# Kernel optimization log

Measured on AMD Instinct MI355X. Metric: run time of the kernel, lower is better.

The kernel has to match this reference:

```python
import jax, jax.numpy as jnp
import numpy as np

NSIDE = 256
N_FACETS = 12 * NSIDE * NSIDE  # 786432
N0 = 300000
N1 = 300000
M = 4194304  # pooled child slots, divisible by 4

JRLL = jnp.array([2, 2, 2, 2, 3, 3, 3, 3, 4, 4, 4, 4], dtype=jnp.int32)
JPLL = jnp.array([1, 3, 5, 7, 0, 2, 4, 6, 1, 3, 5, 7], dtype=jnp.int32)


def _compress_bits(v):
    # keep even bits of v and compact them (de-interleave), 32-bit
    v = v & 0x55555555
    v = (v | (v >> 1)) & 0x33333333
    v = (v | (v >> 2)) & 0x0F0F0F0F
    v = (v | (v >> 4)) & 0x00FF00FF
    v = (v | (v >> 8)) & 0x0000FFFF
    return v


def pix2vec_nest(nside, pix):
    # HEALPix nested pix -> unit cartesian (x, y, z), matches hp.pix2vec(nside, pix, nest=True)
    pix = pix.astype(jnp.int32)
    npface = nside * nside
    face = pix // npface
    ipf = pix - face * npface
    ix = _compress_bits(ipf)
    iy = _compress_bits(ipf >> 1)
    jr = JRLL[face] * nside - ix - iy - 1  # ring index
    north = jr < nside
    south = jr > 3 * nside
    nr = jnp.where(north, jr, jnp.where(south, 4 * nside - jr, nside))
    fact2 = 4.0 / (12.0 * nside * nside)
    fact1 = (2.0 * nside) * fact2
    nrf = nr.astype(jnp.float32)
    z = jnp.where(
        north, 1.0 - nrf * nrf * fact2,
        jnp.where(south, nrf * nrf * fact2 - 1.0,
                  (2 * nside - jr).astype(jnp.float32) * fact1))
    kshift = jnp.where(north | south, 0, (jr - nside) & 1)
    num = JPLL[face] * nr + ix - iy + 1 + kshift
    jp = jnp.where(num >= 0, num // 2, -((-num) // 2))  # C-style truncating division
    jp = jnp.where(jp > 4 * nr, jp - 4 * nr, jp)
    jp = jnp.where(jp < 1, jp + 4 * nr, jp)
    phi = (jp.astype(jnp.float32) - (kshift.astype(jnp.float32) + 1.0) * 0.5) * (jnp.pi * 0.5) / nrf
    sth = jnp.sqrt((1.0 - z) * (1.0 + z))
    return sth * jnp.cos(phi), sth * jnp.sin(phi), z


def _safe_div(num, den):
    # matches torch.nan_to_num(num/den) here because den==0 implies num==0 (scores >= 0)
    d = jnp.where(den == 0, 1.0, den)
    return jnp.where(den == 0, 0.0, num / d)


def center_of_gravity(position, scores):
    # position [M,3], scores [M]; 4 children per parent (view(-1,4) in torch)
    s = scores.reshape(-1, 4)              # [P,4]
    p = position.reshape(-1, 4, 3)         # [P,4,3]
    den = s.sum(axis=1)                    # [P]
    pos_cog = _safe_div(jnp.einsum('pc,pcd->pd', s, p), den[:, None])
    cnt = (s > 0).sum(axis=1).astype(s.dtype)
    score_cog = _safe_div(den, cnt)
    return pos_cog, score_cog


def setup_inputs() -> dict:
    key = jax.random.key(0)
    k1, k2, k3, k4, k5 = jax.random.split(key, 5)
    # unique facet labels per keypoint (mirrors deterministic dict construction)
    img0_child_facets = jax.random.permutation(k1, N_FACETS)[:N0][None].astype(jnp.int32)
    img1_child_facets = jax.random.permutation(k2, N_FACETS)[:N1][None].astype(jnp.int32)
    correspondences = jax.random.randint(k3, (1, N0), 0, N1, dtype=jnp.int32)  # all >= 0
    filt = jax.random.randint(k4, (M,), 0, N_FACETS, dtype=jnp.int32)
    keypointScores1 = jax.random.uniform(k5, (1, N1), dtype=jnp.float32)
    return {
        'nside': NSIDE,
        'correspondences': correspondences,
        'img0_child_facets': img0_child_facets,
        'img1_child_facets': img1_child_facets,
        'img0_filtered_child_facets_for_pooling': filt,
        'keypointScores1': keypointScores1,
    }


def reference(nside, correspondences, img0_child_facets, img1_child_facets,
              img0_filtered_child_facets_for_pooling, keypointScores1):
    # all correspondences >= 0 in this setup -> masked_select keeps everything
    n_kpts0 = correspondences.shape[1]
    kptidx_with_corr_img0 = jnp.arange(n_kpts0, dtype=jnp.int32)
    kptidx_with_corr_img1 = correspondences[0].astype(jnp.int32)
    facets_with_corr_img0 = img0_child_facets[0]                      # [N0]
    facets_with_corr_img1 = img1_child_facets[0][kptidx_with_corr_img1]
    # dict {facet_img0 -> facet_img1}, then {0: 0} override
    lut_corr = (jnp.zeros(N_FACETS, jnp.int32)
                .at[facets_with_corr_img0].set(facets_with_corr_img1.astype(jnp.int32))
                .at[0].set(0))
    # dict {facet_img1 -> keypoint index}, then {0: 0} override
    lut_kpt = (jnp.zeros(N_FACETS, jnp.int32)
               .at[img1_child_facets[0]].set(jnp.arange(img1_child_facets.shape[1], dtype=jnp.int32))
               .at[0].set(0))
    # torch.isin(filtered, facets_with_corr_img0) via membership table
    member = jnp.zeros(N_FACETS, bool).at[facets_with_corr_img0].set(True)
    filt = img0_filtered_child_facets_for_pooling
    mask = member[filt].astype(jnp.float32)                           # [M]
    filt_masked = (filt.astype(jnp.float32) * mask).astype(jnp.int32)
    a = lut_corr[filt_masked]                                         # corresponding img1 facets
    x, y, z = pix2vec_nest(nside, a)
    pos = jnp.stack([x, y, z], axis=1) * mask[:, None]                # [M,3]
    b = lut_kpt[a]
    scores = keypointScores1[0][b] * mask                             # [M]
    pos_cog, score_cog = center_of_gravity(pos, scores)
    return (pos_cog, score_cog[None, :], kptidx_with_corr_img0,
            kptidx_with_corr_img1, keypointScores1)
```

## Files before the change

### kernel.cpp

```cpp
#include <hip/hip_runtime.h>
#include <hip/hip_bf16.h>

#define NSIDE    256
#define NFACETS  786432

typedef int vint4 __attribute__((ext_vector_type(4)));
typedef unsigned uvec4 __attribute__((ext_vector_type(4)));

__device__ __forceinline__ unsigned encode_score(float s) {
    if (s <= 0.f) return 0u;
    unsigned u = __float_as_uint(s);
    u += 0x8000u + ((u >> 16) & 1u);
    int e = (int)((u >> 23) & 0xFFu);
    unsigned m = (u >> 16) & 0x7Fu;
    int field = e - 95;
    if (field < 1)  { field = 1; m = 0u; }
    if (field > 31) { field = 31; m = 127u; }
    return ((unsigned)field << 7) | m;
}
__device__ __forceinline__ float decode_score(unsigned c) {
    if (c == 0u) return 0.f;
    unsigned field = (c >> 7) & 0x1Fu;
    unsigned m = c & 0x7Fu;
    return __uint_as_float(((field + 95u) << 23) | (m << 16));
}

__device__ __forceinline__ unsigned compress_bits(unsigned v) {
    v &= 0x55555555u;
    v = (v | (v >> 1)) & 0x33333333u;
    v = (v | (v >> 2)) & 0x0F0F0F0Fu;
    v = (v | (v >> 4)) & 0x00FF00FFu;
    v = (v | (v >> 8)) & 0x0000FFFFu;
    return v;
}

__device__ __forceinline__ float3 pix2vec_nest256(int pix) {
    int face = pix >> 16;
    unsigned ipf = (unsigned)(pix & 0xFFFF);
    int ix = (int)compress_bits(ipf);
    int iy = (int)compress_bits(ipf >> 1);
    int jrll = 2 + (face >> 2);
    int jpll = 2 * (face & 3) + (((face >> 2) == 1) ? 0 : 1);
    int jr = jrll * NSIDE - ix - iy - 1;
    bool north = jr < NSIDE;
    bool south = jr > 3 * NSIDE;
    int nr = north ? jr : (south ? 4 * NSIDE - jr : NSIDE);
    const float fact2 = 4.0f / (12.0f * (float)NSIDE * (float)NSIDE);
    const float fact1 = (2.0f * (float)NSIDE) * fact2;
    float nrf = (float)nr;
    float z;
    if (north)      z = 1.0f - nrf * nrf * fact2;
    else if (south) z = nrf * nrf * fact2 - 1.0f;
    else            z = (float)(2 * NSIDE - jr) * fact1;
    int kshift = (north || south) ? 0 : (jr & 1);
    int num = jpll * nr + ix - iy + 1 + kshift;
    int jp = num / 2;
    if (jp > 4 * nr) jp -= 4 * nr;
    if (jp < 1)      jp += 4 * nr;
    float phi = ((float)jp - ((float)kshift + 1.0f) * 0.5f) * (1.5707963267948966f / nrf);
    float sth = sqrtf((1.0f - z) * (1.0f + z));
    float sp, cp;
    __sincosf(phi, &sp, &cp);
    float3 r;
    r.x = sth * cp;
    r.y = sth * sp;
    r.z = z;
    return r;
}

__global__ __launch_bounds__(256)
void zero_tail_kernel(uvec4* __restrict__ table4,
                      const int* __restrict__ corr,
                      const float* __restrict__ kps,
                      float* __restrict__ out,
                      int nwords4, int n0, int n1,
                      int idx0_off, int idx1_off, int kps_off) {
    int i = blockIdx.x * blockDim.x + threadIdx.x;
    if (i < nwords4) {
        uvec4 z = {0u, 0u, 0u, 0u};
        table4[i] = z;
    }
    if (i < n0) {
        __builtin_nontemporal_store((float)i, &out[idx0_off + i]);
        __builtin_nontemporal_store((float)corr[i], &out[idx1_off + i]);
    }
    if (i < n1) {
        __builtin_nontemporal_store(kps[i], &out[kps_off + i]);
    }
}

__global__ __launch_bounds__(256)
void build_kernel(const int* __restrict__ corr,
                  const int* __restrict__ f0s,
                  const int* __restrict__ f1s,
                  const float* __restrict__ kps,
                  unsigned* __restrict__ table,
                  int n0) {
    int i = blockIdx.x * blockDim.x + threadIdx.x;
    if (i >= n0) return;
    int f0 = f0s[i];
    int j  = corr[i];
    int a = (f0 == 0) ? 0 : f1s[j];
    int b = (a == 0) ? 0 : j;
    float sc = kps[b];
    unsigned code = ((unsigned)a << 12) | encode_score(sc);
    table[f0] = code;
}

__global__ __launch_bounds__(256)
void cog_kernel(const vint4* __restrict__ filt4,
                const unsigned* __restrict__ table,
                float* __restrict__ out,
                int P, int score_off) {
    int p = blockIdx.x * blockDim.x + threadIdx.x;
    if (p >= P) return;
    vint4 f = __builtin_nontemporal_load(&filt4[p]);
    unsigned t0 = table[f.x];
    unsigned t1 = table[f.y];
    unsigned t2 = table[f.z];
    unsigned t3 = table[f.w];
    float s0 = decode_score(t0 & 0xFFFu);
    float s1 = decode_score(t1 & 0xFFFu);
    float s2 = decode_score(t2 & 0xFFFu);
    float s3 = decode_score(t3 & 0xFFFu);
    float3 v0 = pix2vec_nest256((int)(t0 >> 12));
    float3 v1 = pix2vec_nest256((int)(t1 >> 12));
    float3 v2 = pix2vec_nest256((int)(t2 >> 12));
    float3 v3 = pix2vec_nest256((int)(t3 >> 12));
    float den = s0 + s1 + s2 + s3;
    float px = s0 * v0.x + s1 * v1.x + s2 * v2.x + s3 * v3.x;
    float py = s0 * v0.y + s1 * v1.y + s2 * v2.y + s3 * v3.y;
    float pz = s0 * v0.z + s1 * v1.z + s2 * v2.z + s3 * v3.z;
    int cnt = (int)(s0 > 0.f) + (int)(s1 > 0.f) + (int)(s2 > 0.f) + (int)(s3 > 0.f);
    float ox = 0.f, oy = 0.f, oz = 0.f, osc = 0.f;
    if (den != 0.f) {
        float inv = 1.0f / den;
        ox = px * inv; oy = py * inv; oz = pz * inv;
        float rcp = (cnt == 1) ? 1.f : (cnt == 2) ? 0.5f : (cnt == 3) ? (1.f / 3.f) : 0.25f;
        osc = den * rcp;
    }
    __builtin_nontemporal_store(ox, &out[3 * p + 0]);
    __builtin_nontemporal_store(oy, &out[3 * p + 1]);
    __builtin_nontemporal_store(oz, &out[3 * p + 2]);
    __builtin_nontemporal_store(osc, &out[score_off + p]);
}

extern "C" void kernel_launch(void* const* d_in, const int* in_sizes, int n_in,
                              void* d_out, int out_size, void* d_ws, size_t ws_size,
                              hipStream_t stream) {
    const int* corr = (const int*)d_in[1];
    const int* f0s  = (const int*)d_in[2];
    const int* f1s  = (const int*)d_in[3];
    const int* filt = (const int*)d_in[4];
    const float* kps = (const float*)d_in[5];

    const int n0 = in_sizes[1];
    const int n1 = in_sizes[5];
    const int M  = in_sizes[4];
    const int P  = M / 4;

    const int score_off = 3 * P;
    const int idx0_off  = 4 * P;
    const int idx1_off  = idx0_off + n0;
    const int kps_off   = idx1_off + n0;

    unsigned* table = (unsigned*)d_ws;
    float* out = (float*)d_out;

    const int b = 256;
    const int nwords4 = NFACETS / 4;
    int nmax = nwords4;
    if (n0 > nmax) nmax = n0;
    if (n1 > nmax) nmax = n1;

    zero_tail_kernel<<<(nmax + b - 1) / b, b, 0, stream>>>((uvec4*)table, corr, kps, out,
                                                           nwords4, n0, n1,
                                                           idx0_off, idx1_off, kps_off);
    build_kernel<<<(n0 + b - 1) / b, b, 0, stream>>>(corr, f0s, f1s, kps, table, n0);
    cog_kernel<<<(P + b - 1) / b, b, 0, stream>>>((const vint4*)filt, table, out, P, score_off);
}
```

Before: 44.15 us.

## Add LDS membership bitmap to skip table gathers and pix2vec for empty facets

The build kernel now also sets a bit per occupied facet in a global bitmap (96KB), which the cog kernel copies into shared memory. The cog kernel becomes a persistent grid-stride kernel of 1024-thread blocks. It tests the bitmap before gathering from the 3MB table and skips pix2vec when all four scores are zero. This cuts random global gathers for unmatched facets, at the cost of atomics in the build kernel, a bitmap copy per block, reduced occupancy from the large shared allocation, and lost parallelism from the fixed 256-block grid.

Result: slower. 50.05 us (+13.4%).

```diff
diff --git a/kernel.cpp b/kernel.cpp
--- a/kernel.cpp
+++ b/kernel.cpp
@@ -3,6 +3,7 @@
 
 #define NSIDE    256
 #define NFACETS  786432
+#define BM_WORDS 24576
 
 typedef int vint4 __attribute__((ext_vector_type(4)));
 typedef unsigned uvec4 __attribute__((ext_vector_type(4)));
@@ -69,7 +70,7 @@
 }
 
 __global__ __launch_bounds__(256)
-void zero_tail_kernel(uvec4* __restrict__ table4,
+void zero_tail_kernel(uvec4* __restrict__ ws4,
                       const int* __restrict__ corr,
                       const float* __restrict__ kps,
                       float* __restrict__ out,
@@ -78,7 +79,7 @@
     int i = blockIdx.x * blockDim.x + threadIdx.x;
     if (i < nwords4) {
         uvec4 z = {0u, 0u, 0u, 0u};
-        table4[i] = z;
+        ws4[i] = z;
     }
     if (i < n0) {
         __builtin_nontemporal_store((float)i, &out[idx0_off + i]);
@@ -95,6 +96,7 @@
                   const int* __restrict__ f1s,
                   const float* __restrict__ kps,
                   unsigned* __restrict__ table,
+                  unsigned* __restrict__ gbm,
                   int n0) {
     int i = blockIdx.x * blockDim.x + threadIdx.x;
     if (i >= n0) return;
@@ -105,44 +107,59 @@
     float sc = kps[b];
     unsigned code = ((unsigned)a << 12) | encode_score(sc);
     table[f0] = code;
+    atomicOr(&gbm[f0 >> 5], 1u << (f0 & 31));
 }
 
-__global__ __launch_bounds__(256)
+__global__ __launch_bounds__(1024, 1)
 void cog_kernel(const vint4* __restrict__ filt4,
                 const unsigned* __restrict__ table,
+                const unsigned* __restrict__ gbm,
                 float* __restrict__ out,
                 int P, int score_off) {
-    int p = blockIdx.x * blockDim.x + threadIdx.x;
-    if (p >= P) return;
-    vint4 f = __builtin_nontemporal_load(&filt4[p]);
-    unsigned t0 = table[f.x];
-    unsigned t1 = table[f.y];
-    unsigned t2 = table[f.z];
-    unsigned t3 = table[f.w];
-    float s0 = decode_score(t0 & 0xFFFu);
-    float s1 = decode_score(t1 & 0xFFFu);
-    float s2 = decode_score(t2 & 0xFFFu);
-    float s3 = decode_score(t3 & 0xFFFu);
-    float3 v0 = pix2vec_nest256((int)(t0 >> 12));
-    float3 v1 = pix2vec_nest256((int)(t1 >> 12));
-    float3 v2 = pix2vec_nest256((int)(t2 >> 12));
-    float3 v3 = pix2vec_nest256((int)(t3 >> 12));
-    float den = s0 + s1 + s2 + s3;
-    float px = s0 * v0.x + s1 * v1.x + s2 * v2.x + s3 * v3.x;
-    float py = s0 * v0.y + s1 * v1.y + s2 * v2.y + s3 * v3.y;
-    float pz = s0 * v0.z + s1 * v1.z + s2 * v2.z + s3 * v3.z;
-    int cnt = (int)(s0 > 0.f) + (int)(s1 > 0.f) + (int)(s2 > 0.f) + (int)(s3 > 0.f);
-    float ox = 0.f, oy = 0.f, oz = 0.f, osc = 0.f;
-    if (den != 0.f) {
-        float inv = 1.0f / den;
-        ox = px * inv; oy = py * inv; oz = pz * inv;
-        float rcp = (cnt == 1) ? 1.f : (cnt == 2) ? 0.5f : (cnt == 3) ? (1.f / 3.f) : 0.25f;
-        osc = den * rcp;
+    __shared__ unsigned bm[BM_WORDS];
+    {
+        const uvec4* g4 = (const uvec4*)gbm;
+        uvec4* b4 = (uvec4*)bm;
+        for (int w = threadIdx.x; w < BM_WORDS / 4; w += blockDim.x) b4[w] = g4[w];
     }
-    __builtin_nontemporal_store(ox, &out[3 * p + 0]);
-    __builtin_nontemporal_store(oy, &out[3 * p + 1]);
-    __builtin_nontemporal_store(oz, &out[3 * p + 2]);
-    __builtin_nontemporal_store(osc, &out[score_off + p]);
+    __syncthreads();
+    const int stride = gridDim.x * blockDim.x;
+    for (int p = blockIdx.x * blockDim.x + threadIdx.x; p < P; p += stride) {
+        vint4 f = __builtin_nontemporal_load(&filt4[p]);
+        bool m0 = (bm[f.x >> 5] >> (f.x & 31)) & 1u;
+        bool m1 = (bm[f.y >> 5] >> (f.y & 31)) & 1u;
+        bool m2 = (bm[f.z >> 5] >> (f.z & 31)) & 1u;
+        bool m3 = (bm[f.w >> 5] >> (f.w & 31)) & 1u;
+        unsigned t0 = 0u, t1 = 0u, t2 = 0u, t3 = 0u;
+        if (m0) t0 = table[f.x];
+        if (m1) t1 = table[f.y];
+        if (m2) t2 = table[f.z];
+        if (m3) t3 = table[f.w];
+        float s0 = decode_score(t0 & 0xFFFu);
+        float s1 = decode_score(t1 & 0xFFFu);
+        float s2 = decode_score(t2 & 0xFFFu);
+        float s3 = decode_score(t3 & 0xFFFu);
+        float den = s0 + s1 + s2 + s3;
+        float ox = 0.f, oy = 0.f, oz = 0.f, osc = 0.f;
+        if (den != 0.f) {
+            float3 v0 = pix2vec_nest256((int)(t0 >> 12));
+            float3 v1 = pix2vec_nest256((int)(t1 >> 12));
+            float3 v2 = pix2vec_nest256((int)(t2 >> 12));
+            float3 v3 = pix2vec_nest256((int)(t3 >> 12));
+            float px = s0 * v0.x + s1 * v1.x + s2 * v2.x + s3 * v3.x;
+            float py = s0 * v0.y + s1 * v1.y + s2 * v2.y + s3 * v3.y;
+            float pz = s0 * v0.z + s1 * v1.z + s2 * v2.z + s3 * v3.z;
+            int cnt = (int)(s0 > 0.f) + (int)(s1 > 0.f) + (int)(s2 > 0.f) + (int)(s3 > 0.f);
+            float inv = 1.0f / den;
+            ox = px * inv; oy = py * inv; oz = pz * inv;
+            float rcp = (cnt == 1) ? 1.f : (cnt == 2) ? 0.5f : (cnt == 3) ? (1.f / 3.f) : 0.25f;
+            osc = den * rcp;
+        }
+        __builtin_nontemporal_store(ox, &out[3 * p + 0]);
+        __builtin_nontemporal_store(oy, &out[3 * p + 1]);
+        __builtin_nontemporal_store(oz, &out[3 * p + 2]);
+        __builtin_nontemporal_store(osc, &out[score_off + p]);
+    }
 }
 
 extern "C" void kernel_launch(void* const* d_in, const int* in_sizes, int n_in,
@@ -165,17 +182,18 @@
     const int kps_off   = idx1_off + n0;
 
     unsigned* table = (unsigned*)d_ws;
+    unsigned* gbm   = table + NFACETS;
     float* out = (float*)d_out;
 
     const int b = 256;
-    const int nwords4 = NFACETS / 4;
+    const int nwords4 = (NFACETS + BM_WORDS) / 4;
     int nmax = nwords4;
     if (n0 > nmax) nmax = n0;
     if (n1 > nmax) nmax = n1;
 
-    zero_tail_kernel<<<(nmax + b - 1) / b, b, 0, stream>>>((uvec4*)table, corr, kps, out,
+    zero_tail_kernel<<<(nmax + b - 1) / b, b, 0, stream>>>((uvec4*)d_ws, corr, kps, out,
                                                            nwords4, n0, n1,
                                                            idx0_off, idx1_off, kps_off);
-    build_kernel<<<(n0 + b - 1) / b, b, 0, stream>>>(corr, f0s, f1s, kps, table, n0);
-    cog_kernel<<<(P + b - 1) / b, b, 0, stream>>>((const vint4*)filt, table, out, P, score_off);
+    build_kernel<<<(n0 + b - 1) / b, b, 0, stream>>>(corr, f0s, f1s, kps, table, gbm, n0);
+    cog_kernel<<<256, 1024, 0, stream>>>((const vint4*)filt, table, gbm, out, P, score_off);
 }
```
